# Kernel optimization log

Measured on AMD Instinct MI355X. Metric: run time of the kernel, lower is better.

The kernel has to match this reference:

```python
import jax, jax.numpy as jnp
import numpy as np

MEM_DIM, H, W = 1024, 16, 16
HW = H * W
N_TOKENS, BATCH = 8192, 8
C1, C2, EPS = 0.01, 0.03, 1e-8


def setup_inputs() -> dict:
    key = jax.random.key(0)
    ks = jax.random.split(key, 5)
    std_w = 1.0 / np.sqrt(HW)
    return {
        "input_tokens": jax.random.normal(ks[0], (N_TOKENS, BATCH, HW), dtype=jnp.float32),
        "memory": jax.random.normal(ks[1], (MEM_DIM, H, W), dtype=jnp.float32) * 0.1,
        "Wq": jax.random.normal(ks[2], (HW, HW), dtype=jnp.float32) * std_w,
        "Wk": jax.random.normal(ks[3], (HW, HW), dtype=jnp.float32) * std_w,
        "Wv": jax.random.normal(ks[4], (HW, HW), dtype=jnp.float32) * std_w,
    }


def _ssim(q, k):
    # q: [N, HW], k: [M, HW] -> ssim: [N, M]
    qm = jnp.mean(q, axis=1, keepdims=True)          # [N,1]
    km = jnp.mean(k, axis=1, keepdims=True)          # [M,1]
    qv = jnp.var(q, axis=1, ddof=1, keepdims=True)   # torch.var unbiased
    kv = jnp.var(k, axis=1, ddof=1, keepdims=True)
    cov = ((q - qm) @ (k - km).T) / (HW - 1)         # [N,M]
    mean_prod = qm @ km.T                            # [N,M]
    numerator = (2.0 * mean_prod + C1) * (2.0 * cov + C2)
    denominator = (qm ** 2 + km.T ** 2 + C1) * (qv + kv.T + C2)
    return numerator / (denominator + EPS)


def reference(input_tokens, memory, Wq, Wk, Wv):
    Nt, B, F = input_tokens.shape
    x = input_tokens.reshape(Nt * B, HW)             # [N, HW]
    q = x @ Wq.T                                     # Linear(bias=False): x @ W^T
    m = memory.reshape(MEM_DIM, HW)
    k = m @ Wk.T
    v = m @ Wv.T
    ssim = _ssim(q, k)                               # [N, MEM_DIM]
    att = jax.nn.softmax(ssim, axis=1)
    out = (att @ v).reshape(Nt, B, F)
    return out
```

## Files before the change

kernel.cpp:

```cpp
#include <hip/hip_runtime.h>
#include <math.h>

typedef __attribute__((ext_vector_type(8)))  short bf16x8;
typedef __attribute__((ext_vector_type(16))) float f32x16;

#define MFMA32(a, b, c) __builtin_amdgcn_mfma_f32_32x32x16_bf16((a), (b), (c), 0, 0, 0)

namespace {
constexpr int HWF   = 256;
constexpr int MEMD  = 1024;
constexpr int NROWS = 65536;
constexpr int TM    = 128;
constexpr int TJ    = 64;
constexpr int NT    = MEMD / TJ;
constexpr int THREADS = 512;
constexpr float C1v  = 0.01f;
constexpr float C2v  = 0.03f;
constexpr float EPSv = 1e-8f;
constexpr float RK   = 1.0f / 255.0f;

constexpr int KB0 = 0;
constexpr int KB1 = 32768;
constexpr int VB0 = 65536;
constexpr int VB1 = 98304;
constexpr int PB  = 131072;
constexpr int PSTRIDE = 144;
constexpr int QSTAT = PB + TM * PSTRIDE;
constexpr int QPART = QSTAT + 1024;
constexpr int SMEM_SZ = QPART + 2048;
}

__device__ __forceinline__ short f2bf(float f) {
    union { float f; unsigned u; } v; v.f = f;
    unsigned r = v.u + 0x7fffu + ((v.u >> 16) & 1u);
    return (short)(r >> 16);
}
__device__ __forceinline__ float bf2f(short s) {
    union { unsigned u; float f; } v;
    v.u = ((unsigned)(unsigned short)s) << 16;
    return v.f;
}

__device__ __forceinline__ void dma_tile(const short* gbase, char* smem, int ldsbase,
                                         int wave, int lane) {
    const char* g = (const char*)gbase + wave * 4096 + lane * 16;
    char* l = smem + ldsbase + wave * 4096;
    #pragma unroll
    for (int i = 0; i < 4; ++i) {
        __builtin_amdgcn_global_load_lds(
            (const __attribute__((address_space(1))) unsigned int*)(g + i * 1024),
            (__attribute__((address_space(3))) unsigned int*)(l + i * 1024), 16, 0, 0);
    }
}

__global__ __launch_bounds__(256) void cast_wq(const float* __restrict__ W,
                                               short* __restrict__ Wb) {
    int i = blockIdx.x * 256 + threadIdx.x;
    Wb[i] = f2bf(W[i]);
}

__global__ __launch_bounds__(256) void prep_kv(
    const float* __restrict__ mem, const float* __restrict__ Wk,
    const float* __restrict__ Wv, short* __restrict__ kblob,
    short* __restrict__ vblob, float* __restrict__ km, float* __restrict__ kv)
{
    __shared__ __align__(16) float mrows[4][HWF];
    __shared__ float redS[4][8];
    const int t = threadIdx.x, j0 = blockIdx.x * 4;

    for (int r = 0; r < 4; ++r) mrows[r][t] = mem[(size_t)(j0 + r) * HWF + t];
    __syncthreads();

    const float4* wk4 = reinterpret_cast<const float4*>(Wk + (size_t)t * HWF);
    const float4* wv4 = reinterpret_cast<const float4*>(Wv + (size_t)t * HWF);
    float kt[4] = {0, 0, 0, 0}, vt[4] = {0, 0, 0, 0};
    for (int i = 0; i < 64; ++i) {
        const float4 a = wk4[i], b = wv4[i];
        for (int r = 0; r < 4; ++r) {
            const float4 m = reinterpret_cast<const float4*>(mrows[r])[i];
            kt[r] += m.x * a.x + m.y * a.y + m.z * a.z + m.w * a.w;
            vt[r] += m.x * b.x + m.y * b.y + m.z * b.z + m.w * b.w;
        }
    }

    const int wv_ = t >> 6, ln = t & 63;
    {
        float s[4];
        for (int r = 0; r < 4; ++r) s[r] = kt[r];
        for (int m = 1; m < 64; m <<= 1)
            for (int r = 0; r < 4; ++r) s[r] += __shfl_xor(s[r], m);
        if (ln == 0) {
            for (int r = 0; r < 4; ++r) redS[wv_][r] = s[r];
        }
    }
    __syncthreads();
    float kmv[4], kc4[4];
    for (int r = 0; r < 4; ++r) {
        kmv[r] = (redS[0][r] + redS[1][r] + redS[2][r] + redS[3][r]) * (1.f / HWF);
        kc4[r] = kt[r] - kmv[r];
    }
    {
        float s[4];
        for (int r = 0; r < 4; ++r) s[r] = kc4[r] * kc4[r];
        for (int m = 1; m < 64; m <<= 1)
            for (int r = 0; r < 4; ++r) s[r] += __shfl_xor(s[r], m);
        if (ln == 0) {
            for (int r = 0; r < 4; ++r) redS[wv_][4 + r] = s[r];
        }
    }
    __syncthreads();
    float kvv[4];
    for (int r = 0; r < 4; ++r)
        kvv[r] = (redS[0][4+r] + redS[1][4+r] + redS[2][4+r] + redS[3][4+r]) * (1.f / (HWF - 1));

    const int jt = j0 >> 6;
    for (int r = 0; r < 4; ++r) {
        const int ro = (j0 & 63) + r;
        kblob[jt * 16384 + ro * 256 + (((t >> 3) ^ (ro & 7)) * 8) + (t & 7)] = f2bf(kc4[r]);
        vblob[jt * 16384 + t * 64 + (((ro >> 3) ^ (t & 7)) * 8) + (ro & 7)] = f2bf(vt[r]);
    }
    if (t < 4) { km[j0 + t] = kmv[t]; kv[j0 + t] = kvv[t]; }
}

__global__ __launch_bounds__(THREADS, 2) void attn(
    const float* __restrict__ x, const short* __restrict__ wq_bf,
    const short* __restrict__ kblob, const short* __restrict__ vblob,
    const float* __restrict__ kmg, const float* __restrict__ kvg,
    float* __restrict__ out)
{
    __shared__ __align__(16) char smem[SMEM_SZ];
    const int t = threadIdx.x, wave = t >> 6, lane = t & 63;
    const int lo = lane & 31, hi = lane >> 5;
    const int rg = wave & 3, cs = wave >> 2;
    const int n0 = blockIdx.x * TM;
    const int arow = 32 * rg + lo;

    bf16x8 qA[16];
    {
        const float* xr = x + (size_t)(n0 + arow) * HWF;
        #pragma unroll
        for (int s = 0; s < 16; ++s) {
            const float4 a = *reinterpret_cast<const float4*>(xr + 16 * s + 8 * hi);
            const float4 b = *reinterpret_cast<const float4*>(xr + 16 * s + 8 * hi + 4);
            bf16x8 f;
            f[0]=f2bf(a.x); f[1]=f2bf(a.y); f[2]=f2bf(a.z); f[3]=f2bf(a.w);
            f[4]=f2bf(b.x); f[5]=f2bf(b.y); f[6]=f2bf(b.z); f[7]=f2bf(b.w);
            qA[s] = f;
        }
    }

    f32x16 O4[4];
    #pragma unroll
    for (int i = 0; i < 4; ++i) O4[i] = (f32x16)(0.f);
    #pragma unroll
    for (int nt = 0; nt < 4; ++nt) {
        #pragma unroll
        for (int s = 0; s < 16; ++s) {
            const bf16x8 wb = *reinterpret_cast<const bf16x8*>(
                wq_bf + (size_t)(128 * cs + 32 * nt + lo) * HWF + 16 * s + 8 * hi);
            O4[nt] = MFMA32(qA[s], wb, O4[nt]);
        }
    }

    #pragma unroll
    for (int i = 0; i < 16; ++i) {
        float sv  = O4[0][i] + O4[1][i] + O4[2][i] + O4[3][i];
        float ssv = O4[0][i]*O4[0][i] + O4[1][i]*O4[1][i]
                  + O4[2][i]*O4[2][i] + O4[3][i]*O4[3][i];
        #pragma unroll
        for (int m = 1; m < 32; m <<= 1) { sv += __shfl_xor(sv, m); ssv += __shfl_xor(ssv, m); }
        if (lo == 0) {
            const int row = 32 * rg + (i & 3) + 8 * (i >> 2) + 4 * hi;
            *reinterpret_cast<float2*>(smem + QPART + (row * 2 + cs) * 8) =
                make_float2(sv, ssv);
        }
    }
    #pragma unroll
    for (int nt = 0; nt < 4; ++nt) {
        #pragma unroll
        for (int i = 0; i < 16; ++i) {
            const int row = 32 * rg + (i & 3) + 8 * (i >> 2) + 4 * hi;
            const int k = 128 * cs + 32 * nt + lo;
            *reinterpret_cast<short*>(
                smem + row * 512 + (((k >> 3) ^ (row & 7)) * 16) + (k & 7) * 2) =
                f2bf(O4[nt][i]);
        }
    }
    __syncthreads();

    if (t < TM) {
        const float2 p0 = *reinterpret_cast<float2*>(smem + QPART + (t * 2 + 0) * 8);
        const float2 p1 = *reinterpret_cast<float2*>(smem + QPART + (t * 2 + 1) * 8);
        const float s = p0.x + p1.x, ss = p0.y + p1.y;
        const float qm = s * (1.f / HWF);
        const float qv = (ss - s * s * (1.f / HWF)) * (1.f / (HWF - 1));
        *reinterpret_cast<float2*>(smem + QSTAT + t * 8) = make_float2(qm, qv);
    }
    __syncthreads();

    #pragma unroll
    for (int s = 0; s < 16; ++s)
        qA[s] = *reinterpret_cast<const bf16x8*>(
            smem + arow * 512 + (((2 * s + hi) ^ (arow & 7)) * 16));
    float qm16[16], qv16[16];
    #pragma unroll
    for (int i = 0; i < 16; ++i) {
        const int row = 32 * rg + (i & 3) + 8 * (i >> 2) + 4 * hi;
        const float2 st = *reinterpret_cast<const float2*>(smem + QSTAT + row * 8);
        qm16[i] = st.x; qv16[i] = st.y;
    }
    __syncthreads();

    dma_tile(kblob, smem, KB0, wave, lane);
    dma_tile(vblob, smem, VB0, wave, lane);

    float l16[16];
    #pragma unroll
    for (int i = 0; i < 16; ++i) l16[i] = 0.f;
    #pragma unroll
    for (int i = 0; i < 4; ++i) O4[i] = (f32x16)(0.f);

    const int brow = 32 * cs + lo;

    for (int jt = 0; jt < NT; ++jt) {
        const int cur = jt & 1;
        const int kb = cur ? KB1 : KB0, vb = cur ? VB1 : VB0;
        const int kbn = cur ? KB0 : KB1, vbn = cur ? VB0 : VB1;
        __syncthreads();
        if (jt + 1 < NT) {
            dma_tile(kblob + (size_t)(jt + 1) * 16384, smem, kbn, wave, lane);
            dma_tile(vblob + (size_t)(jt + 1) * 16384, smem, vbn, wave, lane);
        }

        f32x16 sacc = (f32x16)(0.f);
        #pragma unroll
        for (int s = 0; s < 16; ++s) {
            const bf16x8 kfr = *reinterpret_cast<const bf16x8*>(
                smem + kb + brow * 512 + (((2 * s + hi) ^ (brow & 7)) * 16));
            sacc = MFMA32(qA[s], kfr, sacc);
        }

        const int j = 64 * jt + 32 * cs + lo;
        const float km_ = kmg[j], kv_ = kvg[j];
        const float A1 = 2.f * km_, kk1 = km_ * km_ + C1v, kk2 = kv_ + C2v;
        #pragma unroll
        for (int i = 0; i < 16; ++i) {
            const float cov2 = __builtin_fmaf(sacc[i], 2.f * RK, C2v);
            const float num  = __builtin_fmaf(A1, qm16[i], C1v) * cov2;
            const float den  = __builtin_fmaf(
                __builtin_fmaf(qm16[i], qm16[i], kk1), (qv16[i] + kk2), EPSv);
            const float p = __expf(__fdividef(num, den));
            const short pb = f2bf(p);
            l16[i] += bf2f(pb);
            const int row = 32 * rg + (i & 3) + 8 * (i >> 2) + 4 * hi;
            *reinterpret_cast<short*>(smem + PB + row * PSTRIDE + (32 * cs + lo) * 2) = pb;
        }
        __syncthreads();

        bf16x8 pa[4];
        #pragma unroll
        for (int s = 0; s < 4; ++s)
            pa[s] = *reinterpret_cast<const bf16x8*>(
                smem + PB + arow * PSTRIDE + 32 * s + 16 * hi);
        #pragma unroll
        for (int ct = 0; ct < 4; ++ct) {
            const int c = 128 * cs + 32 * ct + lo;
            #pragma unroll
            for (int s = 0; s < 4; ++s) {
                const bf16x8 vfr = *reinterpret_cast<const bf16x8*>(
                    smem + vb + c * 128 + (((2 * s + hi) ^ (c & 7)) * 16));
                O4[ct] = MFMA32(pa[s], vfr, O4[ct]);
            }
        }
    }

    #pragma unroll
    for (int i = 0; i < 16; ++i) {
        float sv = l16[i];
        #pragma unroll
        for (int m = 1; m < 32; m <<= 1) sv += __shfl_xor(sv, m);
        if (lo == 0) {
            const int row = 32 * rg + (i & 3) + 8 * (i >> 2) + 4 * hi;
            *reinterpret_cast<float*>(smem + QPART + (row * 2 + cs) * 4) = sv;
        }
    }
    __syncthreads();
    if (t < TM) {
        const float a = *reinterpret_cast<float*>(smem + QPART + (t * 2 + 0) * 4);
        const float b = *reinterpret_cast<float*>(smem + QPART + (t * 2 + 1) * 4);
        *reinterpret_cast<float*>(smem + QSTAT + t * 4) = 1.f / (a + b);
    }
    __syncthreads();

    #pragma unroll
    for (int ct = 0; ct < 4; ++ct) {
        #pragma unroll
        for (int i = 0; i < 16; ++i) {
            const int row = 32 * rg + (i & 3) + 8 * (i >> 2) + 4 * hi;
            const float rl = *reinterpret_cast<const float*>(smem + QSTAT + row * 4);
            out[(size_t)(n0 + row) * HWF + 128 * cs + 32 * ct + lo] = O4[ct][i] * rl;
        }
    }
}

extern "C" void kernel_launch(void* const* d_in, const int* in_sizes, int n_in,
                              void* d_out, int out_size, void* d_ws, size_t ws_size,
                              hipStream_t stream) {
    (void)in_sizes; (void)n_in; (void)out_size; (void)ws_size;
    const float* x   = (const float*)d_in[0];
    const float* mem = (const float*)d_in[1];
    const float* Wq  = (const float*)d_in[2];
    const float* Wk  = (const float*)d_in[3];
    const float* Wv  = (const float*)d_in[4];
    float* out = (float*)d_out;

    short* wq_bf = (short*)d_ws;
    short* kblob = wq_bf + 65536;
    short* vblob = kblob + (size_t)MEMD * HWF;
    float* km    = (float*)(vblob + (size_t)MEMD * HWF);
    float* kv    = km + MEMD;

    cast_wq<<<256, 256, 0, stream>>>(Wq, wq_bf);
    prep_kv<<<MEMD / 4, 256, 0, stream>>>(mem, Wk, Wv, kblob, vblob, km, kv);
    attn<<<NROWS / TM, THREADS, 0, stream>>>(x, wq_bf, kblob, vblob, km, kv, out);
}
```

Before: 287.5 us.

## Restructure attention so each wave owns full rows, with register-resident P and transposed MFMAs

Each block now takes 256 rows, and every wave handles 32 tokens across all 256 output columns. The old scheme split columns across two wave groups. Q is computed transposed so its row statistics can be reduced within the wave, and P is repacked into MFMA operands in registers using permlane32 swaps. This removes the LDS round trips for Q, P and the row sums, along with most block barriers. Key statistics are precomputed into a float4 blob that is DMA'd to LDS, the first tile prefetch now overlaps the Q projection, and setprio is placed around the MFMA bursts. The cost is much higher register pressure, with 8 output accumulators plus 8 Q accumulators per wave, which may spill or lower occupancy.

```diff
diff --git a/kernel.cpp b/kernel.cpp
--- a/kernel.cpp
+++ b/kernel.cpp
@@ -3,6 +3,7 @@
 
 typedef __attribute__((ext_vector_type(8)))  short bf16x8;
 typedef __attribute__((ext_vector_type(16))) float f32x16;
+typedef __attribute__((ext_vector_type(4)))  unsigned uint4v;
 
 #define MFMA32(a, b, c) __builtin_amdgcn_mfma_f32_32x32x16_bf16((a), (b), (c), 0, 0, 0)
 
@@ -10,9 +11,8 @@
 constexpr int HWF   = 256;
 constexpr int MEMD  = 1024;
 constexpr int NROWS = 65536;
-constexpr int TM    = 128;
-constexpr int TJ    = 64;
-constexpr int NT    = MEMD / TJ;
+constexpr int TM    = 256;
+constexpr int NT    = MEMD / 64;
 constexpr int THREADS = 512;
 constexpr float C1v  = 0.01f;
 constexpr float C2v  = 0.03f;
@@ -23,11 +23,10 @@
 constexpr int KB1 = 32768;
 constexpr int VB0 = 65536;
 constexpr int VB1 = 98304;
-constexpr int PB  = 131072;
-constexpr int PSTRIDE = 144;
-constexpr int QSTAT = PB + TM * PSTRIDE;
-constexpr int QPART = QSTAT + 1024;
-constexpr int SMEM_SZ = QPART + 2048;
+constexpr int SB0 = 131072;
+constexpr int SB1 = 132096;
+constexpr int LRED = 133120;
+constexpr int SMEM_SZ = LRED + 1024;
 }
 
 __device__ __forceinline__ short f2bf(float f) {
@@ -35,10 +34,25 @@
     unsigned r = v.u + 0x7fffu + ((v.u >> 16) & 1u);
     return (short)(r >> 16);
 }
-__device__ __forceinline__ float bf2f(short s) {
-    union { unsigned u; float f; } v;
-    v.u = ((unsigned)(unsigned short)s) << 16;
-    return v.f;
+
+__device__ __forceinline__ unsigned cvtpk(float a, float b) {
+    unsigned r;
+    asm("v_cvt_pk_bf16_f32 %0, %1, %2" : "=v"(r) : "v"(a), "v"(b));
+    return r;
+}
+
+__device__ __forceinline__ void plswap(unsigned &a, unsigned &b) {
+#if defined(__has_builtin) && __has_builtin(__builtin_amdgcn_permlane32_swap)
+    auto r = __builtin_amdgcn_permlane32_swap((int)a, (int)b, false, false);
+    a = (unsigned)r[0]; b = (unsigned)r[1];
+#else
+    const bool h = (threadIdx.x & 32) != 0;
+    const unsigned ax = (unsigned)__shfl_xor((int)a, 32);
+    const unsigned bx = (unsigned)__shfl_xor((int)b, 32);
+    const unsigned na = h ? bx : a;
+    const unsigned nb = h ? b : ax;
+    a = na; b = nb;
+#endif
 }
 
 __device__ __forceinline__ void dma_tile(const short* gbase, char* smem, int ldsbase,
@@ -53,6 +67,14 @@
     }
 }
 
+__device__ __forceinline__ void dma_stats(const float* sblob, char* smem, int sb,
+                                          int jt, int lane) {
+    __builtin_amdgcn_global_load_lds(
+        (const __attribute__((address_space(1))) unsigned int*)
+            ((const char*)sblob + (size_t)jt * 1024 + lane * 16),
+        (__attribute__((address_space(3))) unsigned int*)(smem + sb + lane * 16), 16, 0, 0);
+}
+
 __global__ __launch_bounds__(256) void cast_wq(const float* __restrict__ W,
                                                short* __restrict__ Wb) {
     int i = blockIdx.x * 256 + threadIdx.x;
@@ -62,7 +84,7 @@
 __global__ __launch_bounds__(256) void prep_kv(
     const float* __restrict__ mem, const float* __restrict__ Wk,
     const float* __restrict__ Wv, short* __restrict__ kblob,
-    short* __restrict__ vblob, float* __restrict__ km, float* __restrict__ kv)
+    short* __restrict__ vblob, float4* __restrict__ sblob)
 {
     __shared__ __align__(16) float mrows[4][HWF];
     __shared__ float redS[4][8];
@@ -119,186 +141,172 @@
         kblob[jt * 16384 + ro * 256 + (((t >> 3) ^ (ro & 7)) * 8) + (t & 7)] = f2bf(kc4[r]);
         vblob[jt * 16384 + t * 64 + (((ro >> 3) ^ (t & 7)) * 8) + (ro & 7)] = f2bf(vt[r]);
     }
-    if (t < 4) { km[j0 + t] = kmv[t]; kv[j0 + t] = kvv[t]; }
+    if (t < 4) {
+        sblob[j0 + t] = make_float4(2.f * kmv[t], kmv[t] * kmv[t] + C1v,
+                                    kvv[t] + C2v, 0.f);
+    }
 }
 
 __global__ __launch_bounds__(THREADS, 2) void attn(
     const float* __restrict__ x, const short* __restrict__ wq_bf,
     const short* __restrict__ kblob, const short* __restrict__ vblob,
-    const float* __restrict__ kmg, const float* __restrict__ kvg,
-    float* __restrict__ out)
+    const float* __restrict__ sblob, float* __restrict__ out)
 {
     __shared__ __align__(16) char smem[SMEM_SZ];
     const int t = threadIdx.x, wave = t >> 6, lane = t & 63;
     const int lo = lane & 31, hi = lane >> 5;
-    const int rg = wave & 3, cs = wave >> 2;
+    const int rg = wave;
     const int n0 = blockIdx.x * TM;
-    const int arow = 32 * rg + lo;
-
-    bf16x8 qA[16];
+    const int tok = n0 + 32 * rg + lo;
+
+    dma_tile(kblob, smem, KB0, wave, lane);
+    dma_tile(vblob, smem, VB0, wave, lane);
+    if (wave == 0) dma_stats(sblob, smem, SB0, 0, lane);
+
+    bf16x8 xB[16];
     {
-        const float* xr = x + (size_t)(n0 + arow) * HWF;
+        const float* xr = x + (size_t)tok * HWF;
         #pragma unroll
         for (int s = 0; s < 16; ++s) {
             const float4 a = *reinterpret_cast<const float4*>(xr + 16 * s + 8 * hi);
             const float4 b = *reinterpret_cast<const float4*>(xr + 16 * s + 8 * hi + 4);
-            bf16x8 f;
-            f[0]=f2bf(a.x); f[1]=f2bf(a.y); f[2]=f2bf(a.z); f[3]=f2bf(a.w);
-            f[4]=f2bf(b.x); f[5]=f2bf(b.y); f[6]=f2bf(b.z); f[7]=f2bf(b.w);
-            qA[s] = f;
-        }
-    }
-
-    f32x16 O4[4];
-    #pragma unroll
-    for (int i = 0; i < 4; ++i) O4[i] = (f32x16)(0.f);
-    #pragma unroll
-    for (int nt = 0; nt < 4; ++nt) {
+            uint4v u;
+            u[0] = cvtpk(a.x, a.y); u[1] = cvtpk(a.z, a.w);
+            u[2] = cvtpk(b.x, b.y); u[3] = cvtpk(b.z, b.w);
+            xB[s] = __builtin_bit_cast(bf16x8, u);
+        }
+    }
+
+    f32x16 qD[8];
+    #pragma unroll
+    for (int nt = 0; nt < 8; ++nt) qD[nt] = (f32x16)(0.f);
+    #pragma unroll
+    for (int nt = 0; nt < 8; ++nt) {
         #pragma unroll
         for (int s = 0; s < 16; ++s) {
-            const bf16x8 wb = *reinterpret_cast<const bf16x8*>(
-                wq_bf + (size_t)(128 * cs + 32 * nt + lo) * HWF + 16 * s + 8 * hi);
-            O4[nt] = MFMA32(qA[s], wb, O4[nt]);
-        }
-    }
-
-    #pragma unroll
-    for (int i = 0; i < 16; ++i) {
-        float sv  = O4[0][i] + O4[1][i] + O4[2][i] + O4[3][i];
-        float ssv = O4[0][i]*O4[0][i] + O4[1][i]*O4[1][i]
-                  + O4[2][i]*O4[2][i] + O4[3][i]*O4[3][i];
-        #pragma unroll
-        for (int m = 1; m < 32; m <<= 1) { sv += __shfl_xor(sv, m); ssv += __shfl_xor(ssv, m); }
-        if (lo == 0) {
-            const int row = 32 * rg + (i & 3) + 8 * (i >> 2) + 4 * hi;
-            *reinterpret_cast<float2*>(smem + QPART + (row * 2 + cs) * 8) =
-                make_float2(sv, ssv);
-        }
-    }
-    #pragma unroll
-    for (int nt = 0; nt < 4; ++nt) {
+            const bf16x8 wa = *reinterpret_cast<const bf16x8*>(
+                wq_bf + (size_t)(32 * nt + lo) * HWF + 16 * s + 8 * hi);
+            qD[nt] = MFMA32(wa, xB[s], qD[nt]);
+        }
+    }
+
+    float qs = 0.f, qss = 0.f;
+    #pragma unroll
+    for (int nt = 0; nt < 8; ++nt)
         #pragma unroll
         for (int i = 0; i < 16; ++i) {
-            const int row = 32 * rg + (i & 3) + 8 * (i >> 2) + 4 * hi;
-            const int k = 128 * cs + 32 * nt + lo;
-            *reinterpret_cast<short*>(
-                smem + row * 512 + (((k >> 3) ^ (row & 7)) * 16) + (k & 7) * 2) =
-                f2bf(O4[nt][i]);
-        }
-    }
-    __syncthreads();
-
-    if (t < TM) {
-        const float2 p0 = *reinterpret_cast<float2*>(smem + QPART + (t * 2 + 0) * 8);
-        const float2 p1 = *reinterpret_cast<float2*>(smem + QPART + (t * 2 + 1) * 8);
-        const float s = p0.x + p1.x, ss = p0.y + p1.y;
-        const float qm = s * (1.f / HWF);
-        const float qv = (ss - s * s * (1.f / HWF)) * (1.f / (HWF - 1));
-        *reinterpret_cast<float2*>(smem + QSTAT + t * 8) = make_float2(qm, qv);
-    }
-    __syncthreads();
-
-    #pragma unroll
-    for (int s = 0; s < 16; ++s)
-        qA[s] = *reinterpret_cast<const bf16x8*>(
-            smem + arow * 512 + (((2 * s + hi) ^ (arow & 7)) * 16));
-    float qm16[16], qv16[16];
-    #pragma unroll
-    for (int i = 0; i < 16; ++i) {
-        const int row = 32 * rg + (i & 3) + 8 * (i >> 2) + 4 * hi;
-        const float2 st = *reinterpret_cast<const float2*>(smem + QSTAT + row * 8);
-        qm16[i] = st.x; qv16[i] = st.y;
-    }
-    __syncthreads();
-
-    dma_tile(kblob, smem, KB0, wave, lane);
-    dma_tile(vblob, smem, VB0, wave, lane);
-
-    float l16[16];
-    #pragma unroll
-    for (int i = 0; i < 16; ++i) l16[i] = 0.f;
-    #pragma unroll
-    for (int i = 0; i < 4; ++i) O4[i] = (f32x16)(0.f);
-
-    const int brow = 32 * cs + lo;
+            const float v = qD[nt][i];
+            qs += v; qss = __builtin_fmaf(v, v, qss);
+        }
+    qs += __shfl_xor(qs, 32);
+    qss += __shfl_xor(qss, 32);
+    const float qm  = qs * (1.f / HWF);
+    const float qv  = (qss - qs * qs * (1.f / HWF)) * (1.f / (HWF - 1));
+    const float qm2 = qm * qm;
+
+    bf16x8 qA[16];
+    #pragma unroll
+    for (int nt = 0; nt < 8; ++nt) {
+        unsigned w[8];
+        #pragma unroll
+        for (int p = 0; p < 8; ++p) w[p] = cvtpk(qD[nt][2 * p], qD[nt][2 * p + 1]);
+        #pragma unroll
+        for (int h = 0; h < 2; ++h) {
+            unsigned a0 = w[4 * h + 0], b0 = w[4 * h + 2];
+            unsigned a1 = w[4 * h + 1], b1 = w[4 * h + 3];
+            plswap(a0, b0); plswap(a1, b1);
+            uint4v u; u[0] = a0; u[1] = a1; u[2] = b0; u[3] = b1;
+            qA[2 * nt + h] = __builtin_bit_cast(bf16x8, u);
+        }
+    }
+
+    f32x16 O4[8];
+    #pragma unroll
+    for (int ct = 0; ct < 8; ++ct) O4[ct] = (f32x16)(0.f);
+    float l = 0.f;
+    const int rx = (lo & 7);
 
     for (int jt = 0; jt < NT; ++jt) {
         const int cur = jt & 1;
-        const int kb = cur ? KB1 : KB0, vb = cur ? VB1 : VB0;
-        const int kbn = cur ? KB0 : KB1, vbn = cur ? VB0 : VB1;
+        const int kb = cur ? KB1 : KB0, vb = cur ? VB1 : VB0, sb = cur ? SB1 : SB0;
+        const int kbn = cur ? KB0 : KB1, vbn = cur ? VB0 : VB1, sbn = cur ? SB0 : SB1;
         __syncthreads();
         if (jt + 1 < NT) {
             dma_tile(kblob + (size_t)(jt + 1) * 16384, smem, kbn, wave, lane);
             dma_tile(vblob + (size_t)(jt + 1) * 16384, smem, vbn, wave, lane);
-        }
-
-        f32x16 sacc = (f32x16)(0.f);
-        #pragma unroll
-        for (int s = 0; s < 16; ++s) {
-            const bf16x8 kfr = *reinterpret_cast<const bf16x8*>(
-                smem + kb + brow * 512 + (((2 * s + hi) ^ (brow & 7)) * 16));
-            sacc = MFMA32(qA[s], kfr, sacc);
-        }
-
-        const int j = 64 * jt + 32 * cs + lo;
-        const float km_ = kmg[j], kv_ = kvg[j];
-        const float A1 = 2.f * km_, kk1 = km_ * km_ + C1v, kk2 = kv_ + C2v;
-        #pragma unroll
-        for (int i = 0; i < 16; ++i) {
-            const float cov2 = __builtin_fmaf(sacc[i], 2.f * RK, C2v);
-            const float num  = __builtin_fmaf(A1, qm16[i], C1v) * cov2;
-            const float den  = __builtin_fmaf(
-                __builtin_fmaf(qm16[i], qm16[i], kk1), (qv16[i] + kk2), EPSv);
-            const float p = __expf(__fdividef(num, den));
-            const short pb = f2bf(p);
-            l16[i] += bf2f(pb);
-            const int row = 32 * rg + (i & 3) + 8 * (i >> 2) + 4 * hi;
-            *reinterpret_cast<short*>(smem + PB + row * PSTRIDE + (32 * cs + lo) * 2) = pb;
-        }
-        __syncthreads();
-
-        bf16x8 pa[4];
-        #pragma unroll
-        for (int s = 0; s < 4; ++s)
-            pa[s] = *reinterpret_cast<const bf16x8*>(
-                smem + PB + arow * PSTRIDE + 32 * s + 16 * hi);
-        #pragma unroll
-        for (int ct = 0; ct < 4; ++ct) {
-            const int c = 128 * cs + 32 * ct + lo;
+            if (wave == 0) dma_stats(sblob, smem, sbn, jt + 1, lane);
+        }
+
+        #pragma unroll
+        for (int jh = 0; jh < 2; ++jh) {
+            f32x16 sacc = (f32x16)(0.f);
+            __builtin_amdgcn_s_setprio(1);
             #pragma unroll
-            for (int s = 0; s < 4; ++s) {
-                const bf16x8 vfr = *reinterpret_cast<const bf16x8*>(
-                    smem + vb + c * 128 + (((2 * s + hi) ^ (c & 7)) * 16));
-                O4[ct] = MFMA32(pa[s], vfr, O4[ct]);
+            for (int s = 0; s < 16; ++s) {
+                const bf16x8 kfr = *reinterpret_cast<const bf16x8*>(
+                    smem + kb + jh * 16384 + lo * 512 + (((2 * s + hi) ^ rx) * 16));
+                sacc = MFMA32(kfr, qA[s], sacc);
             }
-        }
-    }
-
-    #pragma unroll
-    for (int i = 0; i < 16; ++i) {
-        float sv = l16[i];
-        #pragma unroll
-        for (int m = 1; m < 32; m <<= 1) sv += __shfl_xor(sv, m);
-        if (lo == 0) {
-            const int row = 32 * rg + (i & 3) + 8 * (i >> 2) + 4 * hi;
-            *reinterpret_cast<float*>(smem + QPART + (row * 2 + cs) * 4) = sv;
-        }
-    }
-    __syncthreads();
-    if (t < TM) {
-        const float a = *reinterpret_cast<float*>(smem + QPART + (t * 2 + 0) * 4);
-        const float b = *reinterpret_cast<float*>(smem + QPART + (t * 2 + 1) * 4);
-        *reinterpret_cast<float*>(smem + QSTAT + t * 4) = 1.f / (a + b);
-    }
-    __syncthreads();
-
-    #pragma unroll
-    for (int ct = 0; ct < 4; ++ct) {
+            __builtin_amdgcn_s_setprio(0);
+
+            unsigned pw[8];
+            #pragma unroll
+            for (int p = 0; p < 8; ++p) {
+                float pr[2];
+                #pragma unroll
+                for (int q = 0; q < 2; ++q) {
+                    const int i = 2 * p + q;
+                    const float4 st = *reinterpret_cast<const float4*>(
+                        smem + sb + hi * 64 + ((32 * jh + (i & 3) + 8 * (i >> 2)) * 16));
+                    const float cov2 = __builtin_fmaf(sacc[i], 2.f * RK, C2v);
+                    const float num  = __builtin_fmaf(st.x, qm, C1v) * cov2;
+                    const float den  = __builtin_fmaf(qm2 + st.y, qv + st.z, EPSv);
+                    pr[q] = __expf(__fdividef(num, den));
+                    l += pr[q];
+                }
+                pw[p] = cvtpk(pr[0], pr[1]);
+            }
+
+            #pragma unroll
+            for (int h = 0; h < 2; ++h) {
+                const int ks = 2 * jh + h;
+                unsigned a0 = pw[4 * h + 0], b0 = pw[4 * h + 2];
+                unsigned a1 = pw[4 * h + 1], b1 = pw[4 * h + 3];
+                plswap(a0, b0); plswap(a1, b1);
+                uint4v u; u[0] = a0; u[1] = a1; u[2] = b0; u[3] = b1;
+                const bf16x8 pa = __builtin_bit_cast(bf16x8, u);
+                __builtin_amdgcn_s_setprio(1);
+                #pragma unroll
+                for (int ct = 0; ct < 8; ++ct) {
+                    const bf16x8 vfr = *reinterpret_cast<const bf16x8*>(
+                        smem + vb + (32 * ct + lo) * 128 + (((2 * ks + hi) ^ rx) * 16));
+                    O4[ct] = MFMA32(pa, vfr, O4[ct]);
+                }
+                __builtin_amdgcn_s_setprio(0);
+            }
+        }
+    }
+
+    const float lf = l + __shfl_xor(l, 32);
+    if (hi == 0)
+        *reinterpret_cast<float*>(smem + LRED + (wave * 32 + lo) * 4) = lf;
+    float rl[16];
+    #pragma unroll
+    for (int g = 0; g < 4; ++g) {
+        const float4 lv = *reinterpret_cast<const float4*>(
+            smem + LRED + wave * 128 + (8 * g + 4 * hi) * 4);
+        rl[4 * g + 0] = 1.f / lv.x;
+        rl[4 * g + 1] = 1.f / lv.y;
+        rl[4 * g + 2] = 1.f / lv.z;
+        rl[4 * g + 3] = 1.f / lv.w;
+    }
+
+    #pragma unroll
+    for (int ct = 0; ct < 8; ++ct) {
         #pragma unroll
         for (int i = 0; i < 16; ++i) {
             const int row = 32 * rg + (i & 3) + 8 * (i >> 2) + 4 * hi;
-            const float rl = *reinterpret_cast<const float*>(smem + QSTAT + row * 4);
-            out[(size_t)(n0 + row) * HWF + 128 * cs + 32 * ct + lo] = O4[ct][i] * rl;
+            out[(size_t)(n0 + row) * HWF + 32 * ct + lo] = O4[ct][i] * rl[i];
         }
     }
 }
@@ -317,10 +325,10 @@
     short* wq_bf = (short*)d_ws;
     short* kblob = wq_bf + 65536;
     short* vblob = kblob + (size_t)MEMD * HWF;
-    float* km    = (float*)(vblob + (size_t)MEMD * HWF);
-    float* kv    = km + MEMD;
+    float4* sblob = (float4*)(vblob + (size_t)MEMD * HWF);
 
     cast_wq<<<256, 256, 0, stream>>>(Wq, wq_bf);
-    prep_kv<<<MEMD / 4, 256, 0, stream>>>(mem, Wk, Wv, kblob, vblob, km, kv);
-    attn<<<NROWS / TM, THREADS, 0, stream>>>(x, wq_bf, kblob, vblob, km, kv, out);
-}
+    prep_kv<<<MEMD / 4, 256, 0, stream>>>(mem, Wk, Wv, kblob, vblob, sblob);
+    attn<<<NROWS / TM, THREADS, 0, stream>>>(x, wq_bf, kblob, vblob,
+                                             (const float*)sblob, out);
+}
```

Result: faster. 278.8 us (-3.0%).
